# Performance work log

Hardware: AMD Instinct MI355X
Metric: run time of the kernel (lower is better)

The kernel has to match this reference:

```python
import jax, jax.numpy as jnp
import numpy as np

BN_EPS = 1e-5
GRID_W = 17  # conv output width hardcoded via lat_idx*17+lon_idx

def _conv(x, w, b, stride):
    y = jax.lax.conv_general_dilated(x, w, (stride, stride), [(1, 1), (1, 1)],
                                     dimension_numbers=("NCHW", "OIHW", "NCHW"))
    return y + b[None, :, None, None]

def _bn_eval(x, g, b):
    # running_mean=0, running_var=1 (fresh BatchNorm in eval mode)
    inv = jnp.float32(1.0 / np.sqrt(1.0 + BN_EPS))
    return x * (g[None, :, None, None] * inv) + b[None, :, None, None]

def setup_inputs() -> dict:
    key = jax.random.key(0)
    ks = iter(jax.random.split(key, 64))
    def rn(shape, s=0.05):
        return jax.random.normal(next(ks), shape, jnp.float32) * s
    B, S, K = 512, 128, 64
    NR = 100000
    inp = {}
    inp["roads"] = jax.random.randint(next(ks), (B, S), 0, NR)
    inp["ratios"] = jax.random.uniform(next(ks), (B, S), jnp.float32) * 0.9 + 0.1
    inp["T"] = jax.random.normal(next(ks), (1, 1, 138, 138), jnp.float32)
    inp["lon_idx"] = jax.random.randint(next(ks), (B, K), 0, 17)
    inp["lat_idx"] = jax.random.randint(next(ks), (B, K), 0, 17)
    inp["lengths"] = jax.random.uniform(next(ks), (NR,), jnp.float32) * 100.0 + 1.0
    inp["map_u"] = jnp.arange(NR, dtype=jnp.int32)
    inp["map_s1"] = jax.random.randint(next(ks), (NR,), 0, 14)
    inp["map_s2"] = jax.random.randint(next(ks), (NR,), 0, 7)
    inp["map_s3"] = jax.random.randint(next(ks), (NR,), 0, 2)
    inp["emb_u"] = rn((NR, 128))
    inp["emb_s1"] = rn((14, 16)); inp["emb_s2"] = rn((7, 8)); inp["emb_s3"] = rn((2, 4))
    inp["rho_w1"] = rn((156, 512)); inp["rho_b1"] = jnp.zeros((512,), jnp.float32)
    inp["rho_w21"] = rn((512, 128)); inp["rho_b21"] = jnp.zeros((128,), jnp.float32)
    inp["conv1_w"] = rn((32, 1, 5, 5)); inp["conv1_b"] = jnp.zeros((32,), jnp.float32)
    inp["bn1_g"] = jnp.ones((32,), jnp.float32); inp["bn1_b"] = jnp.zeros((32,), jnp.float32)
    inp["conv2_w"] = rn((64, 32, 4, 4)); inp["conv2_b"] = jnp.zeros((64,), jnp.float32)
    inp["bn2_g"] = jnp.ones((64,), jnp.float32); inp["bn2_b"] = jnp.zeros((64,), jnp.float32)
    inp["conv3_w"] = rn((128, 64, 4, 4)); inp["conv3_b"] = jnp.zeros((128,), jnp.float32)
    inp["bn3_g"] = jnp.ones((128,), jnp.float32); inp["bn3_b"] = jnp.zeros((128,), jnp.float32)
    inp["f2_w1"] = rn((128, 256)); inp["f2_b1"] = jnp.zeros((256,), jnp.float32)
    inp["f2_w2"] = rn((256, 128)); inp["f2_b2"] = jnp.zeros((128,), jnp.float32)
    inp["f_w1"] = rn((256, 512)); inp["f_b1"] = jnp.zeros((512,), jnp.float32)
    inp["f_w21"] = rn((512, 1)); inp["f_b21"] = jnp.zeros((1,), jnp.float32)
    inp["f_w22"] = rn((512, 1)); inp["f_b22"] = jnp.zeros((1,), jnp.float32)
    return inp

def reference(roads, ratios, T, lon_idx, lat_idx, lengths, map_u, map_s1, map_s2, map_s3,
              emb_u, emb_s1, emb_s2, emb_s3, rho_w1, rho_b1, rho_w21, rho_b21,
              conv1_w, conv1_b, bn1_g, bn1_b, conv2_w, conv2_b, bn2_g, bn2_b,
              conv3_w, conv3_b, bn3_g, bn3_b, f2_w1, f2_b1, f2_w2, f2_b2,
              f_w1, f_b1, f_w21, f_b21, f_w22, f_b22):
    # road lengths / weights
    road_lens = lengths[roads] * ratios               # (B,S)
    l = road_lens.sum(axis=1)                         # (B,)
    w = road_lens / l[:, None]                        # (B,S)
    # ProbRho (eval: dropout=id, reparameterize -> mu)
    u = emb_u[map_u[roads]]                           # (B,S,128)
    s1 = emb_s1[map_s1[roads]]; s2 = emb_s2[map_s2[roads]]; s3 = emb_s3[map_s3[roads]]
    x = jnp.concatenate([u, s1, s2, s3], axis=2)      # (B,S,156)
    h = jax.nn.relu(x @ rho_w1 + rho_b1)
    rho = h @ rho_w21 + rho_b21                       # (B,S,128)
    # ProbTraffic_spatial conv stack
    t = jax.nn.leaky_relu(_bn_eval(_conv(T, conv1_w, conv1_b, 2), bn1_g, bn1_b), 0.1)
    t = jax.nn.leaky_relu(_bn_eval(_conv(t, conv2_w, conv2_b, 2), bn2_g, bn2_b), 0.1)
    t = jax.nn.leaky_relu(_bn_eval(_conv(t, conv3_w, conv3_b, 2), bn3_g, bn3_b), 0.1)  # (1,128,17,17)
    c_flat = jnp.transpose(t[0], (1, 2, 0)).reshape(-1, t.shape[1])  # (289,128)
    # fused segment gather + mean over each trajectory's grid cells
    idx = lat_idx * GRID_W + lon_idx                  # (B,K)
    c_mean = c_flat[idx].mean(axis=1)                 # (B,128)
    h2 = jax.nn.selu(c_mean @ f2_w1 + f2_b1)
    c2 = h2 @ f2_w2 + f2_b2                           # (B,128)
    # ProbTravelTime
    xcat = jnp.concatenate([rho, jnp.broadcast_to(c2[:, None, :], rho.shape)], axis=2)  # (B,S,256)
    h3 = jax.nn.relu(xcat @ f_w1 + f_b1)              # (B,S,512)
    logm = (h3 @ f_w21 + f_b21)[..., 0]               # (B,S)
    logv = (h3 @ f_w22 + f_b22)[..., 0]
    logw = jnp.log(w)
    logm_agg = jax.nn.logsumexp(logm + logw, axis=1)
    logv_agg = jax.nn.logsumexp(logv + 2.0 * logw, axis=1)
    logl = jnp.log(l)
    logmu = logl - logm_agg
    loglam = logl - 3.0 * logm_agg - logv_agg
    return (logmu, loglam)
```

## Files before the change

kernel.cpp:

```cpp
#include <hip/hip_runtime.h>
#include <hip/hip_bf16.h>
#include <math.h>

#define BB 512
#define SS 128
#define NROWS (BB*SS)
#define TMG 128
#define NBLKG (NROWS/TMG)

__device__ __forceinline__ float leaky01(float x){ return x >= 0.f ? x : 0.1f*x; }

#define BN_INV 0.9999950000374997f
#define SELU_A 1.6732632423543772f
#define SELU_S 1.0507009873554805f

typedef __attribute__((ext_vector_type(8))) short short8;
typedef __attribute__((ext_vector_type(4))) float f32x4;

__device__ __forceinline__ unsigned short f2bf(float f) {
    unsigned int u = __float_as_uint(f);
    u += 0x7fff + ((u >> 16) & 1);
    return (unsigned short)(u >> 16);
}
__device__ __forceinline__ unsigned int pk2(float a, float b) {
    __hip_bfloat162 h = __float22bfloat162_rn(make_float2(a, b));
    unsigned int u;
    __builtin_memcpy(&u, &h, 4);
    return u;
}
__device__ __forceinline__ uint2 pack4bf(float a, float b, float c, float d) {
    uint2 r; r.x = pk2(a, b); r.y = pk2(c, d); return r;
}

__device__ __forceinline__ unsigned short* xsp(unsigned short* base, int row, int col) {
    unsigned off = (unsigned)(row*384 + col*2);
    off ^= (unsigned)((row & 7) << 4);
    return (unsigned short*)((char*)base + off);
}
__device__ __forceinline__ unsigned short* h1p(unsigned short* base, int row, int col) {
    unsigned off = (unsigned)(row*1024 + col*2);
    off ^= (unsigned)((row & 7) << 4);
    return (unsigned short*)((char*)base + off);
}
__device__ __forceinline__ unsigned short* xcp(unsigned short* base, int row, int col) {
    unsigned off = (unsigned)(row*256 + col*2);
    off ^= (unsigned)((row & 7) << 4);
    return (unsigned short*)((char*)base + off);
}

#define PREP_N (278528 + 32768 + 131072)
#define PREP_BLOCKS (PREP_N/256)
#define CONV1_BLOCKS 578

__global__ __launch_bounds__(256) void combo1_kernel(
    const float* __restrict__ w1, const float* __restrict__ w21, const float* __restrict__ fw1,
    unsigned short* __restrict__ sw1, unsigned short* __restrict__ sw21, unsigned short* __restrict__ sw3,
    const float* __restrict__ c2w_in, const float* __restrict__ c3w_in,
    float* __restrict__ w2t, float* __restrict__ w3t,
    const float* __restrict__ T, const float* __restrict__ cw,
    const float* __restrict__ cbias, const float* __restrict__ g,
    const float* __restrict__ bb, float* __restrict__ out)
{
    if (blockIdx.x < PREP_BLOCKS) {
        int t = blockIdx.x*256 + threadIdx.x;
        if (t < 81920) {
            int j = t & 7; int r = t >> 3; int lane = r & 63; r >>= 6;
            int ks = r % 5; int nt = r / 5;
            int n = nt*16 + (lane & 15);
            int k = ks*32 + (lane >> 4)*8 + j;
            float v = (k < 156) ? w1[k*512 + n] : 0.f;
            sw1[t] = f2bf(v);
        } else if (t < 147456) {
            int u = t - 81920;
            int j = u & 7; int r = u >> 3; int lane = r & 63; r >>= 6;
            int ks = r & 15; int nt = r >> 4;
            int d = nt*16 + (lane & 15);
            int k = ks*32 + (lane >> 4)*8 + j;
            sw21[u] = f2bf(w21[k*128 + d]);
        } else if (t < 278528) {
            int u = t - 147456;
            int j = u & 7; int r = u >> 3; int lane = r & 63; r >>= 6;
            int ks = r & 7; int nt = r >> 3;
            int n = nt*16 + (lane & 15);
            int k = ks*32 + (lane >> 4)*8 + j;
            sw3[u] = f2bf(fw1[k*512 + n]);
        } else if (t < 278528 + 32768) {
            int u = t - 278528;
            int oc = u >> 9; int r = u & 511;
            int kk = r >> 5; int ic = r & 31;
            w2t[u] = c2w_in[oc*512 + ic*16 + kk];
        } else {
            int u = t - (278528 + 32768);
            int oc = u >> 10; int r = u & 1023;
            int kk = r >> 6; int ic = r & 63;
            w3t[u] = c3w_in[oc*1024 + ic*16 + kk];
        }
    } else {
        int t = (blockIdx.x - PREP_BLOCKS)*256 + threadIdx.x;
        if (t >= 32*68*68) return;
        int oc  = t & 31;
        int pos = t >> 5;
        int oy = pos / 68, ox = pos % 68;
        float acc = cbias[oc];
        #pragma unroll
        for (int ky=0; ky<5; ++ky) {
            int iy = oy*2 - 1 + ky;
            if (iy < 0 || iy >= 138) continue;
            #pragma unroll
            for (int kx=0; kx<5; ++kx) {
                int ix = ox*2 - 1 + kx;
                if (ix < 0 || ix >= 138) continue;
                acc += cw[oc*25 + ky*5 + kx] * T[iy*138 + ix];
            }
        }
        acc = acc * (g[oc]*BN_INV) + bb[oc];
        out[pos*32 + oc] = leaky01(acc);
    }
}

__global__ __launch_bounds__(256) void conv2_kernel(
    const float* __restrict__ in,
    const float* __restrict__ w2t,
    const float* __restrict__ bias, const float* __restrict__ g,
    const float* __restrict__ bb, float* __restrict__ out)
{
    int gid = blockIdx.x*256 + threadIdx.x;
    if (gid >= 64*34*34*4) return;
    int icg = gid & 3;
    int o   = gid >> 2;
    int oc  = o & 63;
    int pos = o >> 6;
    int oy = pos / 34, ox = pos % 34;
    float acc = 0.f;
    #pragma unroll
    for (int ky=0; ky<4; ++ky) {
        int iy = oy*2 - 1 + ky;
        if (iy < 0 || iy >= 68) continue;
        #pragma unroll
        for (int kx=0; kx<4; ++kx) {
            int ix = ox*2 - 1 + kx;
            if (ix < 0 || ix >= 68) continue;
            const float* ip = &in[(iy*68+ix)*32 + icg*8];
            const float* wp = &w2t[oc*512 + (ky*4+kx)*32 + icg*8];
            float4 i0 = *(const float4*)ip, i1 = *(const float4*)(ip+4);
            float4 w0 = *(const float4*)wp, w1v = *(const float4*)(wp+4);
            acc += i0.x*w0.x + i0.y*w0.y + i0.z*w0.z + i0.w*w0.w
                 + i1.x*w1v.x + i1.y*w1v.y + i1.z*w1v.z + i1.w*w1v.w;
        }
    }
    acc += __shfl_xor(acc, 1, 64);
    acc += __shfl_xor(acc, 2, 64);
    if (icg == 0) {
        acc = (acc + bias[oc]) * (g[oc]*BN_INV) + bb[oc];
        out[pos*64 + oc] = leaky01(acc);
    }
}

__global__ __launch_bounds__(256) void conv3_kernel(
    const float* __restrict__ in,
    const float* __restrict__ w3t,
    const float* __restrict__ bias, const float* __restrict__ g,
    const float* __restrict__ bb, float* __restrict__ outT)
{
    int gid = blockIdx.x*256 + threadIdx.x;
    if (gid >= 128*289*8) return;
    int icg = gid & 7;
    int o   = gid >> 3;
    int oc  = o & 127;
    int pos = o >> 7;
    int oy = pos / 17, ox = pos % 17;
    float acc = 0.f;
    #pragma unroll
    for (int ky=0; ky<4; ++ky) {
        int iy = oy*2 - 1 + ky;
        if (iy < 0 || iy >= 34) continue;
        #pragma unroll
        for (int kx=0; kx<4; ++kx) {
            int ix = ox*2 - 1 + kx;
            if (ix < 0 || ix >= 34) continue;
            const float* ip = &in[(iy*34+ix)*64 + icg*8];
            const float* wp = &w3t[oc*1024 + (ky*4+kx)*64 + icg*8];
            float4 i0 = *(const float4*)ip, i1 = *(const float4*)(ip+4);
            float4 w0 = *(const float4*)wp, w1v = *(const float4*)(wp+4);
            acc += i0.x*w0.x + i0.y*w0.y + i0.z*w0.z + i0.w*w0.w
                 + i1.x*w1v.x + i1.y*w1v.y + i1.z*w1v.z + i1.w*w1v.w;
        }
    }
    acc += __shfl_xor(acc, 1, 64);
    acc += __shfl_xor(acc, 2, 64);
    acc += __shfl_xor(acc, 4, 64);
    if (icg == 0) {
        acc = (acc + bias[oc]) * (g[oc]*BN_INV) + bb[oc];
        outT[pos*128 + oc] = leaky01(acc);
    }
}

__global__ __launch_bounds__(256) void cmh2c2_kernel(
    const float* __restrict__ t3T, const int* __restrict__ lat, const int* __restrict__ lon,
    const float* __restrict__ w1, const float* __restrict__ b1,
    const float* __restrict__ w2, const float* __restrict__ b2,
    const float* __restrict__ fw1, const float* __restrict__ fb1,
    float* __restrict__ cvb)
{
    __shared__ int   ps[64];
    __shared__ float part[256];
    __shared__ float cms[128];
    __shared__ float h2s[256];
    __shared__ float c2s[128];
    const int b = blockIdx.x;
    const int tid = threadIdx.x;
    if (tid < 64) ps[tid] = lat[b*64+tid]*17 + lon[b*64+tid];
    __syncthreads();
    {
        int d = tid & 127, half = tid >> 7;
        float s = 0.f;
        #pragma unroll 8
        for (int k=0; k<32; ++k) s += t3T[ps[half*32+k]*128 + d];
        part[tid] = s;
    }
    __syncthreads();
    if (tid < 128) cms[tid] = (part[tid] + part[tid+128]) * (1.f/64.f);
    __syncthreads();
    {
        float acc = b1[tid];
        #pragma unroll 8
        for (int k=0; k<128; ++k) acc += cms[k] * w1[k*256 + tid];
        h2s[tid] = acc > 0.f ? SELU_S*acc : SELU_S*SELU_A*(expf(acc)-1.f);
    }
    __syncthreads();
    {
        int d = tid & 127, half = tid >> 7;
        float acc = 0.f;
        #pragma unroll 8
        for (int k=0; k<128; ++k) acc += h2s[half*128 + k] * w2[(half*128+k)*128 + d];
        part[tid] = acc;
    }
    __syncthreads();
    if (tid < 128) c2s[tid] = part[tid] + part[tid+128] + b2[tid];
    __syncthreads();
    {
        float a0 = fb1[tid], a1 = fb1[tid + 256];
        #pragma unroll 8
        for (int k=0; k<128; ++k) {
            float c = c2s[k];
            a0 += c * fw1[(128+k)*512 + tid];
            a1 += c * fw1[(128+k)*512 + 256 + tid];
        }
        cvb[b*512 + tid]       = a0;
        cvb[b*512 + 256 + tid] = a1;
    }
}

__global__ __launch_bounds__(1024, 4) void mega_kernel(
    const int* __restrict__ roads, const float* __restrict__ ratios,
    const float* __restrict__ lengths,
    const int* __restrict__ map_u, const int* __restrict__ map_s1,
    const int* __restrict__ map_s2, const int* __restrict__ map_s3,
    const float* __restrict__ emb_u, const float* __restrict__ emb_s1,
    const float* __restrict__ emb_s2, const float* __restrict__ emb_s3,
    const unsigned short* __restrict__ sw1, const float* __restrict__ b1,
    const unsigned short* __restrict__ sw21, const float* __restrict__ b21,
    const unsigned short* __restrict__ sw3, const float* __restrict__ cvb,
    const float* __restrict__ fw21, const float* __restrict__ fb21,
    const float* __restrict__ fw22, const float* __restrict__ fb22,
    float* __restrict__ out)
{
    __shared__ unsigned short buf[65536];
    float* pmv = (float*)buf;
    float* fin = (float*)buf + 4096;

    const int tid  = threadIdx.x;
    const int wid  = tid >> 6;
    const int lane = tid & 63;
    const int lo   = lane & 15;
    const int hi   = lane >> 4;
    const int b    = blockIdx.x;
    const int r0   = b * TMG;
    const int nt2  = wid >> 1;
    const int rh   = wid & 1;

    short8 afp00 = *(const short8*)&sw1[((wid*2+0)*5 + 0)*512 + lane*8];
    short8 afp10 = *(const short8*)&sw1[((wid*2+1)*5 + 0)*512 + lane*8];
    short8 afp01 = *(const short8*)&sw1[((wid*2+0)*5 + 1)*512 + lane*8];
    short8 afp11 = *(const short8*)&sw1[((wid*2+1)*5 + 1)*512 + lane*8];

    {
        int row = tid >> 3, seg = tid & 7;
        int road = roads[r0 + row];
        const float* src = emb_u + (long)map_u[road]*128 + seg*16;
        #pragma unroll
        for (int i=0;i<4;++i) {
            float4 v = *(const float4*)&src[i*4];
            *(uint2*)xsp(buf, row, seg*16 + i*4) = pack4bf(v.x, v.y, v.z, v.w);
        }
    }
    for (int idx = tid; idx < 128*32; idx += 1024) {
        int row = idx >> 5, k2 = idx & 31;
        int road = roads[r0 + row];
        float v;
        if      (k2 < 16) v = emb_s1[map_s1[road]*16 + k2];
        else if (k2 < 24) v = emb_s2[map_s2[road]*8  + (k2-16)];
        else if (k2 < 28) v = emb_s3[map_s3[road]*4  + (k2-24)];
        else              v = 0.f;
        *xsp(buf, row, 128 + k2) = f2bf(v);
    }
    __syncthreads();

    f32x4 acc1[2][8];
    {
        #pragma unroll
        for (int mt=0;mt<2;++mt)
            #pragma unroll
            for (int rg=0;rg<8;++rg) acc1[mt][rg]=(f32x4)(0.f);
        short8 a0c = afp00, a1c = afp10, a0n = afp01, a1n = afp11;
        #pragma unroll
        for (int ks=0; ks<5; ++ks) {
            short8 a0f = a0c, a1f = a1c;
            if (ks < 3) {
                a0f = *(const short8*)&sw1[((wid*2+0)*5 + ks+2)*512 + lane*8];
                a1f = *(const short8*)&sw1[((wid*2+1)*5 + ks+2)*512 + lane*8];
            }
            const int kb = ks*32 + hi*8;
            short8 bf[4];
            #pragma unroll
            for (int rg=0;rg<4;++rg) bf[rg] = *(const short8*)xsp(buf, rg*16+lo, kb);
            #pragma unroll
            for (int rg=0;rg<4;++rg) {
                acc1[0][rg] = __builtin_amdgcn_mfma_f32_16x16x32_bf16(a0c, bf[rg], acc1[0][rg], 0,0,0);
                acc1[1][rg] = __builtin_amdgcn_mfma_f32_16x16x32_bf16(a1c, bf[rg], acc1[1][rg], 0,0,0);
            }
            #pragma unroll
            for (int rg=0;rg<4;++rg) bf[rg] = *(const short8*)xsp(buf, (4+rg)*16+lo, kb);
            #pragma unroll
            for (int rg=0;rg<4;++rg) {
                acc1[0][4+rg] = __builtin_amdgcn_mfma_f32_16x16x32_bf16(a0c, bf[rg], acc1[0][4+rg], 0,0,0);
                acc1[1][4+rg] = __builtin_amdgcn_mfma_f32_16x16x32_bf16(a1c, bf[rg], acc1[1][4+rg], 0,0,0);
            }
            a0c = a0n; a1c = a1n; a0n = a0f; a1n = a1f;
        }
    }
    __syncthreads();

    short8 a2q0, a2q1, a2q2, a2q3;
    {
        a2q0 = *(const short8*)&sw21[(nt2*16 + 0)*512 + lane*8];
        a2q1 = *(const short8*)&sw21[(nt2*16 + 1)*512 + lane*8];
        a2q2 = *(const short8*)&sw21[(nt2*16 + 2)*512 + lane*8];
        a2q3 = *(const short8*)&sw21[(nt2*16 + 3)*512 + lane*8];
        const int n0 = wid * 32;
        #pragma unroll
        for (int mt=0;mt<2;++mt) {
            const int nb = n0 + mt*16 + hi*4;
            float4 bias = *(const float4*)&b1[nb];
            const float* bp = (const float*)&bias;
            #pragma unroll
            for (int rg=0;rg<8;++rg) {
                const float* a = (const float*)&acc1[mt][rg];
                float y0 = fmaxf(a[0]+bp[0], 0.f), y1 = fmaxf(a[1]+bp[1], 0.f);
                float y2 = fmaxf(a[2]+bp[2], 0.f), y3 = fmaxf(a[3]+bp[3], 0.f);
                *(uint2*)h1p(buf, rg*16+lo, nb) = pack4bf(y0,y1,y2,y3);
            }
        }
    }
    __syncthreads();

    f32x4 acc2[4];
    {
        #pragma unroll
        for (int i=0;i<4;++i) acc2[i]=(f32x4)(0.f);
        #pragma unroll
        for (int ks=0; ks<16; ++ks) {
            short8 a_use = a2q0;
            a2q0 = a2q1; a2q1 = a2q2; a2q2 = a2q3;
            if (ks < 12)
                a2q3 = *(const short8*)&sw21[(nt2*16 + ks+4)*512 + lane*8];
            const int kb = ks*32 + hi*8;
            short8 bf[4];
            #pragma unroll
            for (int i=0;i<4;++i) bf[i] = *(const short8*)h1p(buf, (rh*4+i)*16+lo, kb);
            #pragma unroll
            for (int i=0;i<4;++i)
                acc2[i] = __builtin_amdgcn_mfma_f32_16x16x32_bf16(a_use, bf[i], acc2[i], 0,0,0);
        }
    }
    __syncthreads();

    short8 a3c0, a3c1, a3n0, a3n1;
    {
        a3c0 = *(const short8*)&sw3[((wid*2+0)*8 + 0)*512 + lane*8];
        a3c1 = *(const short8*)&sw3[((wid*2+1)*8 + 0)*512 + lane*8];
        a3n0 = *(const short8*)&sw3[((wid*2+0)*8 + 1)*512 + lane*8];
        a3n1 = *(const short8*)&sw3[((wid*2+1)*8 + 1)*512 + lane*8];
        const int nb = nt2*16 + hi*4;
        float4 bias = *(const float4*)&b21[nb];
        const float* bp = (const float*)&bias;
        #pragma unroll
        for (int i=0;i<4;++i) {
            const float* a = (const float*)&acc2[i];
            *(uint2*)xcp(buf, (rh*4+i)*16+lo, nb) =
                pack4bf(a[0]+bp[0], a[1]+bp[1], a[2]+bp[2], a[3]+bp[3]);
        }
    }
    __syncthreads();

    float sm[8], sv[8];
    {
        const int n0 = wid * 32;
        f32x4 acc[2][8];
        #pragma unroll
        for (int mt=0;mt<2;++mt)
            #pragma unroll
            for (int rg=0;rg<8;++rg) acc[mt][rg]=(f32x4)(0.f);
        #pragma unroll
        for (int ks=0; ks<4; ++ks) {
            short8 c0f = a3c0, c1f = a3c1;
            if (ks < 2) {
                c0f = *(const short8*)&sw3[((wid*2+0)*8 + ks+2)*512 + lane*8];
                c1f = *(const short8*)&sw3[((wid*2+1)*8 + ks+2)*512 + lane*8];
            }
            const int kb = ks*32 + hi*8;
            short8 bf[4];
            #pragma unroll
            for (int rg=0;rg<4;++rg) bf[rg] = *(const short8*)xcp(buf, rg*16+lo, kb);
            #pragma unroll
            for (int rg=0;rg<4;++rg) {
                acc[0][rg] = __builtin_amdgcn_mfma_f32_16x16x32_bf16(a3c0, bf[rg], acc[0][rg], 0,0,0);
                acc[1][rg] = __builtin_amdgcn_mfma_f32_16x16x32_bf16(a3c1, bf[rg], acc[1][rg], 0,0,0);
            }
            #pragma unroll
            for (int rg=0;rg<4;++rg) bf[rg] = *(const short8*)xcp(buf, (4+rg)*16+lo, kb);
            #pragma unroll
            for (int rg=0;rg<4;++rg) {
                acc[0][4+rg] = __builtin_amdgcn_mfma_f32_16x16x32_bf16(a3c0, bf[rg], acc[0][4+rg], 0,0,0);
                acc[1][4+rg] = __builtin_amdgcn_mfma_f32_16x16x32_bf16(a3c1, bf[rg], acc[1][4+rg], 0,0,0);
            }
            a3c0 = a3n0; a3c1 = a3n1; a3n0 = c0f; a3n1 = c1f;
        }
        #pragma unroll
        for (int rg=0;rg<8;++rg){ sm[rg]=0.f; sv[rg]=0.f; }
        #pragma unroll
        for (int mt=0;mt<2;++mt) {
            const int nb = n0 + mt*16 + hi*4;
            float4 bias = *(const float4*)&cvb[b*512 + nb];
            float4 wm   = *(const float4*)&fw21[nb];
            float4 wv   = *(const float4*)&fw22[nb];
            const float *bp=(const float*)&bias, *wmp=(const float*)&wm, *wvp=(const float*)&wv;
            #pragma unroll
            for (int rg=0;rg<8;++rg) {
                const float* a = (const float*)&acc[mt][rg];
                #pragma unroll
                for (int j=0;j<4;++j) {
                    float y = fmaxf(a[j]+bp[j], 0.f);
                    sm[rg] += y*wmp[j];
                    sv[rg] += y*wvp[j];
                }
            }
        }
        #pragma unroll
        for (int rg=0;rg<8;++rg) {
            sm[rg] += __shfl_xor(sm[rg], 16, 64); sm[rg] += __shfl_xor(sm[rg], 32, 64);
            sv[rg] += __shfl_xor(sv[rg], 16, 64); sv[rg] += __shfl_xor(sv[rg], 32, 64);
        }
    }
    __syncthreads();
    if (hi == 0) {
        #pragma unroll
        for (int rg=0;rg<8;++rg) {
            pmv[wid*128 + rg*16 + lo]        = sm[rg];
            pmv[2048 + wid*128 + rg*16 + lo] = sv[rg];
        }
    }
    __syncthreads();

    float rl = 0.f, am = 0.f, av = 0.f;
    if (tid < 128) {
        float s_m = 0.f, s_v = 0.f;
        #pragma unroll
        for (int w=0; w<16; ++w) {
            s_m += pmv[w*128 + tid];
            s_v += pmv[2048 + w*128 + tid];
        }
        s_m += fb21[0]; s_v += fb22[0];
        int gi = r0 + tid;
        rl = lengths[roads[gi]] * ratios[gi];
        float ws = rl;
        #pragma unroll
        for (int off=32; off; off>>=1) ws += __shfl_xor(ws, off, 64);
        if (lane == 0) fin[wid] = ws;
        am = s_m; av = s_v;
    }
    __syncthreads();
    if (tid < 128) {
        float l = fin[0] + fin[1];
        float logl = logf(l);
        float lw = logf(rl) - logl;
        am += lw; av += 2.f*lw;
        float mm = am, mv = av;
        #pragma unroll
        for (int off=32; off; off>>=1) { mm = fmaxf(mm, __shfl_xor(mm, off, 64)); mv = fmaxf(mv, __shfl_xor(mv, off, 64)); }
        if (lane == 0) { fin[2+wid] = mm; fin[4+wid] = mv; fin[8+wid] = logl; }
    }
    __syncthreads();
    if (tid < 128) {
        float mm = fmaxf(fin[2], fin[3]);
        float mv = fmaxf(fin[4], fin[5]);
        float se = expf(am - mm), sev = expf(av - mv);
        #pragma unroll
        for (int off=32; off; off>>=1) { se += __shfl_xor(se, off, 64); sev += __shfl_xor(sev, off, 64); }
        if (lane == 0) { fin[10+wid] = se; fin[12+wid] = sev; }
    }
    __syncthreads();
    if (tid == 0) {
        float mm = fmaxf(fin[2], fin[3]);
        float mv = fmaxf(fin[4], fin[5]);
        float lsem = logf(fin[10] + fin[11]) + mm;
        float lsev = logf(fin[12] + fin[13]) + mv;
        float logl = fin[8];
        out[b]       = logl - lsem;
        out[512 + b] = logl - 3.f*lsem - lsev;
    }
}

extern "C" void kernel_launch(void* const* d_in, const int* in_sizes, int n_in,
                              void* d_out, int out_size, void* d_ws, size_t ws_size,
                              hipStream_t stream) {
    const int*   roads   = (const int*)  d_in[0];
    const float* ratios  = (const float*)d_in[1];
    const float* T       = (const float*)d_in[2];
    const int*   lon_idx = (const int*)  d_in[3];
    const int*   lat_idx = (const int*)  d_in[4];
    const float* lengths = (const float*)d_in[5];
    const int*   map_u   = (const int*)  d_in[6];
    const int*   map_s1  = (const int*)  d_in[7];
    const int*   map_s2  = (const int*)  d_in[8];
    const int*   map_s3  = (const int*)  d_in[9];
    const float* emb_u   = (const float*)d_in[10];
    const float* emb_s1  = (const float*)d_in[11];
    const float* emb_s2  = (const float*)d_in[12];
    const float* emb_s3  = (const float*)d_in[13];
    const float* rho_w1  = (const float*)d_in[14];
    const float* rho_b1  = (const float*)d_in[15];
    const float* rho_w21 = (const float*)d_in[16];
    const float* rho_b21 = (const float*)d_in[17];
    const float* conv1_w = (const float*)d_in[18];
    const float* conv1_b = (const float*)d_in[19];
    const float* bn1_g   = (const float*)d_in[20];
    const float* bn1_b   = (const float*)d_in[21];
    const float* conv2_w = (const float*)d_in[22];
    const float* conv2_b = (const float*)d_in[23];
    const float* bn2_g   = (const float*)d_in[24];
    const float* bn2_b   = (const float*)d_in[25];
    const float* conv3_w = (const float*)d_in[26];
    const float* conv3_b = (const float*)d_in[27];
    const float* bn3_g   = (const float*)d_in[28];
    const float* bn3_b   = (const float*)d_in[29];
    const float* f2_w1   = (const float*)d_in[30];
    const float* f2_b1   = (const float*)d_in[31];
    const float* f2_w2   = (const float*)d_in[32];
    const float* f2_b2   = (const float*)d_in[33];
    const float* f_w1    = (const float*)d_in[34];
    const float* f_b1    = (const float*)d_in[35];
    const float* f_w21   = (const float*)d_in[36];
    const float* f_b21   = (const float*)d_in[37];
    const float* f_w22   = (const float*)d_in[38];
    const float* f_b22   = (const float*)d_in[39];

    float* ws    = (float*)d_ws;
    float* t1    = ws;
    float* t2    = t1 + 147968;
    float* t3T   = t2 + 73984;
    float* cvb   = t3T + 36992;
    float* w2t   = cvb + 262144;
    float* w3t   = w2t + 32768;
    unsigned short* sw1  = (unsigned short*)(w3t + 131072);
    unsigned short* sw21 = sw1 + 81920;
    unsigned short* sw3  = sw21 + 65536;

    combo1_kernel<<<PREP_BLOCKS + CONV1_BLOCKS, 256, 0, stream>>>(
        rho_w1, rho_w21, f_w1, sw1, sw21, sw3,
        conv2_w, conv3_w, w2t, w3t,
        T, conv1_w, conv1_b, bn1_g, bn1_b, t1);
    conv2_kernel<<<(64*34*34*4 + 255)/256, 256, 0, stream>>>(t1, w2t, conv2_b, bn2_g, bn2_b, t2);
    conv3_kernel<<<(128*289*8 + 255)/256, 256, 0, stream>>>(t2, w3t, conv3_b, bn3_g, bn3_b, t3T);
    cmh2c2_kernel<<<512, 256, 0, stream>>>(t3T, lat_idx, lon_idx, f2_w1, f2_b1, f2_w2, f2_b2,
                                           f_w1, f_b1, cvb);
    mega_kernel<<<NBLKG, 1024, 0, stream>>>(roads, ratios, lengths,
                                            map_u, map_s1, map_s2, map_s3,
                                            emb_u, emb_s1, emb_s2, emb_s3,
                                            sw1, rho_b1, sw21, rho_b21,
                                            sw3, cvb, f_w21, f_b21, f_w22, f_b22,
                                            (float*)d_out);
}
```

Measured before the change: 117.1 us.

## Fuse conv and context prep kernels into one cooperative kernel with grid syncs

Merges the weight-prep/conv1, conv2, conv3 and context-MLP kernels into a single cooperative kernel of 256 blocks by 512 threads. Grid-stride loops cover each stage, and grid.sync separates the dependent stages. The goal is to remove three kernel launch boundaries and their drain/fill gaps, at the cost of grid-wide barriers and fewer resident threads per conv stage. The change also relaxes mega_kernel's launch-bounds occupancy hint from 4 to 2, which can change its register allocation, and switches embedding gathers to nontemporal loads.

```diff
diff --git a/kernel.cpp b/kernel.cpp
--- a/kernel.cpp
+++ b/kernel.cpp
@@ -1,6 +1,9 @@
 #include <hip/hip_runtime.h>
 #include <hip/hip_bf16.h>
+#include <hip/hip_cooperative_groups.h>
 #include <math.h>
+
+namespace cg = cooperative_groups;
 
 #define BB 512
 #define SS 128
@@ -48,210 +51,213 @@
     return (unsigned short*)((char*)base + off);
 }
 
-#define PREP_N (278528 + 32768 + 131072)
-#define PREP_BLOCKS (PREP_N/256)
-#define CONV1_BLOCKS 578
-
-__global__ __launch_bounds__(256) void combo1_kernel(
+#define PREP_N 442368
+#define C1_N   147968
+#define C2_N   (64*34*34*4)
+#define C3_N   (128*289*8)
+#define GRID_T (256*512)
+
+__global__ __launch_bounds__(512) void fused_pre_kernel(
     const float* __restrict__ w1, const float* __restrict__ w21, const float* __restrict__ fw1,
     unsigned short* __restrict__ sw1, unsigned short* __restrict__ sw21, unsigned short* __restrict__ sw3,
     const float* __restrict__ c2w_in, const float* __restrict__ c3w_in,
     float* __restrict__ w2t, float* __restrict__ w3t,
-    const float* __restrict__ T, const float* __restrict__ cw,
-    const float* __restrict__ cbias, const float* __restrict__ g,
-    const float* __restrict__ bb, float* __restrict__ out)
+    const float* __restrict__ T, const float* __restrict__ c1w,
+    const float* __restrict__ c1b, const float* __restrict__ g1, const float* __restrict__ bb1,
+    float* __restrict__ t1,
+    const float* __restrict__ c2bias, const float* __restrict__ g2, const float* __restrict__ bb2,
+    float* __restrict__ t2,
+    const float* __restrict__ c3bias, const float* __restrict__ g3, const float* __restrict__ bb3,
+    float* __restrict__ t3T,
+    const int* __restrict__ lat, const int* __restrict__ lon,
+    const float* __restrict__ f2w1, const float* __restrict__ f2b1,
+    const float* __restrict__ f2w2, const float* __restrict__ f2b2,
+    const float* __restrict__ fb1, float* __restrict__ cvb)
 {
-    if (blockIdx.x < PREP_BLOCKS) {
-        int t = blockIdx.x*256 + threadIdx.x;
-        if (t < 81920) {
-            int j = t & 7; int r = t >> 3; int lane = r & 63; r >>= 6;
+    cg::grid_group grid = cg::this_grid();
+    const int tid = threadIdx.x;
+    const int gt  = blockIdx.x*512 + tid;
+
+    __shared__ int   pss[128];
+    __shared__ float cms[256];
+    __shared__ float h2s[512];
+    __shared__ float part[512];
+    __shared__ float c2s[256];
+
+    for (int i = gt; i < PREP_N + C1_N; i += GRID_T) {
+        if (i < 81920) {
+            int j = i & 7; int r = i >> 3; int lane = r & 63; r >>= 6;
             int ks = r % 5; int nt = r / 5;
             int n = nt*16 + (lane & 15);
             int k = ks*32 + (lane >> 4)*8 + j;
             float v = (k < 156) ? w1[k*512 + n] : 0.f;
-            sw1[t] = f2bf(v);
-        } else if (t < 147456) {
-            int u = t - 81920;
+            sw1[i] = f2bf(v);
+        } else if (i < 147456) {
+            int u = i - 81920;
             int j = u & 7; int r = u >> 3; int lane = r & 63; r >>= 6;
             int ks = r & 15; int nt = r >> 4;
             int d = nt*16 + (lane & 15);
             int k = ks*32 + (lane >> 4)*8 + j;
             sw21[u] = f2bf(w21[k*128 + d]);
-        } else if (t < 278528) {
-            int u = t - 147456;
+        } else if (i < 278528) {
+            int u = i - 147456;
             int j = u & 7; int r = u >> 3; int lane = r & 63; r >>= 6;
             int ks = r & 7; int nt = r >> 3;
             int n = nt*16 + (lane & 15);
             int k = ks*32 + (lane >> 4)*8 + j;
             sw3[u] = f2bf(fw1[k*512 + n]);
-        } else if (t < 278528 + 32768) {
-            int u = t - 278528;
+        } else if (i < 278528 + 32768) {
+            int u = i - 278528;
             int oc = u >> 9; int r = u & 511;
             int kk = r >> 5; int ic = r & 31;
             w2t[u] = c2w_in[oc*512 + ic*16 + kk];
-        } else {
-            int u = t - (278528 + 32768);
+        } else if (i < PREP_N) {
+            int u = i - (278528 + 32768);
             int oc = u >> 10; int r = u & 1023;
             int kk = r >> 6; int ic = r & 63;
             w3t[u] = c3w_in[oc*1024 + ic*16 + kk];
-        }
-    } else {
-        int t = (blockIdx.x - PREP_BLOCKS)*256 + threadIdx.x;
-        if (t >= 32*68*68) return;
-        int oc  = t & 31;
-        int pos = t >> 5;
-        int oy = pos / 68, ox = pos % 68;
-        float acc = cbias[oc];
-        #pragma unroll
-        for (int ky=0; ky<5; ++ky) {
+        } else {
+            int t = i - PREP_N;
+            int oc  = t & 31;
+            int pos = t >> 5;
+            int oy = pos / 68, ox = pos % 68;
+            float acc = c1b[oc];
+            #pragma unroll
+            for (int ky=0; ky<5; ++ky) {
+                int iy = oy*2 - 1 + ky;
+                if (iy < 0 || iy >= 138) continue;
+                #pragma unroll
+                for (int kx=0; kx<5; ++kx) {
+                    int ix = ox*2 - 1 + kx;
+                    if (ix < 0 || ix >= 138) continue;
+                    acc += c1w[oc*25 + ky*5 + kx] * T[iy*138 + ix];
+                }
+            }
+            acc = acc * (g1[oc]*BN_INV) + bb1[oc];
+            t1[pos*32 + oc] = leaky01(acc);
+        }
+    }
+    grid.sync();
+
+    for (int gid = gt; gid < C2_N; gid += GRID_T) {
+        int icg = gid & 3;
+        int o   = gid >> 2;
+        int oc  = o & 63;
+        int pos = o >> 6;
+        int oy = pos / 34, ox = pos % 34;
+        float acc = 0.f;
+        #pragma unroll
+        for (int ky=0; ky<4; ++ky) {
             int iy = oy*2 - 1 + ky;
-            if (iy < 0 || iy >= 138) continue;
-            #pragma unroll
-            for (int kx=0; kx<5; ++kx) {
+            if (iy < 0 || iy >= 68) continue;
+            #pragma unroll
+            for (int kx=0; kx<4; ++kx) {
                 int ix = ox*2 - 1 + kx;
-                if (ix < 0 || ix >= 138) continue;
-                acc += cw[oc*25 + ky*5 + kx] * T[iy*138 + ix];
-            }
-        }
-        acc = acc * (g[oc]*BN_INV) + bb[oc];
-        out[pos*32 + oc] = leaky01(acc);
-    }
-}
-
-__global__ __launch_bounds__(256) void conv2_kernel(
-    const float* __restrict__ in,
-    const float* __restrict__ w2t,
-    const float* __restrict__ bias, const float* __restrict__ g,
-    const float* __restrict__ bb, float* __restrict__ out)
-{
-    int gid = blockIdx.x*256 + threadIdx.x;
-    if (gid >= 64*34*34*4) return;
-    int icg = gid & 3;
-    int o   = gid >> 2;
-    int oc  = o & 63;
-    int pos = o >> 6;
-    int oy = pos / 34, ox = pos % 34;
-    float acc = 0.f;
-    #pragma unroll
-    for (int ky=0; ky<4; ++ky) {
-        int iy = oy*2 - 1 + ky;
-        if (iy < 0 || iy >= 68) continue;
-        #pragma unroll
-        for (int kx=0; kx<4; ++kx) {
-            int ix = ox*2 - 1 + kx;
-            if (ix < 0 || ix >= 68) continue;
-            const float* ip = &in[(iy*68+ix)*32 + icg*8];
-            const float* wp = &w2t[oc*512 + (ky*4+kx)*32 + icg*8];
-            float4 i0 = *(const float4*)ip, i1 = *(const float4*)(ip+4);
-            float4 w0 = *(const float4*)wp, w1v = *(const float4*)(wp+4);
-            acc += i0.x*w0.x + i0.y*w0.y + i0.z*w0.z + i0.w*w0.w
-                 + i1.x*w1v.x + i1.y*w1v.y + i1.z*w1v.z + i1.w*w1v.w;
-        }
-    }
-    acc += __shfl_xor(acc, 1, 64);
-    acc += __shfl_xor(acc, 2, 64);
-    if (icg == 0) {
-        acc = (acc + bias[oc]) * (g[oc]*BN_INV) + bb[oc];
-        out[pos*64 + oc] = leaky01(acc);
-    }
-}
-
-__global__ __launch_bounds__(256) void conv3_kernel(
-    const float* __restrict__ in,
-    const float* __restrict__ w3t,
-    const float* __restrict__ bias, const float* __restrict__ g,
-    const float* __restrict__ bb, float* __restrict__ outT)
-{
-    int gid = blockIdx.x*256 + threadIdx.x;
-    if (gid >= 128*289*8) return;
-    int icg = gid & 7;
-    int o   = gid >> 3;
-    int oc  = o & 127;
-    int pos = o >> 7;
-    int oy = pos / 17, ox = pos % 17;
-    float acc = 0.f;
-    #pragma unroll
-    for (int ky=0; ky<4; ++ky) {
-        int iy = oy*2 - 1 + ky;
-        if (iy < 0 || iy >= 34) continue;
-        #pragma unroll
-        for (int kx=0; kx<4; ++kx) {
-            int ix = ox*2 - 1 + kx;
-            if (ix < 0 || ix >= 34) continue;
-            const float* ip = &in[(iy*34+ix)*64 + icg*8];
-            const float* wp = &w3t[oc*1024 + (ky*4+kx)*64 + icg*8];
-            float4 i0 = *(const float4*)ip, i1 = *(const float4*)(ip+4);
-            float4 w0 = *(const float4*)wp, w1v = *(const float4*)(wp+4);
-            acc += i0.x*w0.x + i0.y*w0.y + i0.z*w0.z + i0.w*w0.w
-                 + i1.x*w1v.x + i1.y*w1v.y + i1.z*w1v.z + i1.w*w1v.w;
-        }
-    }
-    acc += __shfl_xor(acc, 1, 64);
-    acc += __shfl_xor(acc, 2, 64);
-    acc += __shfl_xor(acc, 4, 64);
-    if (icg == 0) {
-        acc = (acc + bias[oc]) * (g[oc]*BN_INV) + bb[oc];
-        outT[pos*128 + oc] = leaky01(acc);
-    }
-}
-
-__global__ __launch_bounds__(256) void cmh2c2_kernel(
-    const float* __restrict__ t3T, const int* __restrict__ lat, const int* __restrict__ lon,
-    const float* __restrict__ w1, const float* __restrict__ b1,
-    const float* __restrict__ w2, const float* __restrict__ b2,
-    const float* __restrict__ fw1, const float* __restrict__ fb1,
-    float* __restrict__ cvb)
-{
-    __shared__ int   ps[64];
-    __shared__ float part[256];
-    __shared__ float cms[128];
-    __shared__ float h2s[256];
-    __shared__ float c2s[128];
-    const int b = blockIdx.x;
-    const int tid = threadIdx.x;
-    if (tid < 64) ps[tid] = lat[b*64+tid]*17 + lon[b*64+tid];
-    __syncthreads();
+                if (ix < 0 || ix >= 68) continue;
+                const float* ip = &t1[(iy*68+ix)*32 + icg*8];
+                const float* wp = &w2t[oc*512 + (ky*4+kx)*32 + icg*8];
+                float4 i0 = *(const float4*)ip, i1 = *(const float4*)(ip+4);
+                float4 w0 = *(const float4*)wp, w1v = *(const float4*)(wp+4);
+                acc += i0.x*w0.x + i0.y*w0.y + i0.z*w0.z + i0.w*w0.w
+                     + i1.x*w1v.x + i1.y*w1v.y + i1.z*w1v.z + i1.w*w1v.w;
+            }
+        }
+        acc += __shfl_xor(acc, 1, 64);
+        acc += __shfl_xor(acc, 2, 64);
+        if (icg == 0) {
+            acc = (acc + c2bias[oc]) * (g2[oc]*BN_INV) + bb2[oc];
+            t2[pos*64 + oc] = leaky01(acc);
+        }
+    }
+    grid.sync();
+
+    for (int gid = gt; gid < C3_N; gid += GRID_T) {
+        int icg = gid & 7;
+        int o   = gid >> 3;
+        int oc  = o & 127;
+        int pos = o >> 7;
+        int oy = pos / 17, ox = pos % 17;
+        float acc = 0.f;
+        #pragma unroll
+        for (int ky=0; ky<4; ++ky) {
+            int iy = oy*2 - 1 + ky;
+            if (iy < 0 || iy >= 34) continue;
+            #pragma unroll
+            for (int kx=0; kx<4; ++kx) {
+                int ix = ox*2 - 1 + kx;
+                if (ix < 0 || ix >= 34) continue;
+                const float* ip = &t2[(iy*34+ix)*64 + icg*8];
+                const float* wp = &w3t[oc*1024 + (ky*4+kx)*64 + icg*8];
+                float4 i0 = *(const float4*)ip, i1 = *(const float4*)(ip+4);
+                float4 w0 = *(const float4*)wp, w1v = *(const float4*)(wp+4);
+                acc += i0.x*w0.x + i0.y*w0.y + i0.z*w0.z + i0.w*w0.w
+                     + i1.x*w1v.x + i1.y*w1v.y + i1.z*w1v.z + i1.w*w1v.w;
+            }
+        }
+        acc += __shfl_xor(acc, 1, 64);
+        acc += __shfl_xor(acc, 2, 64);
+        acc += __shfl_xor(acc, 4, 64);
+        if (icg == 0) {
+            acc = (acc + c3bias[oc]) * (g3[oc]*BN_INV) + bb3[oc];
+            t3T[pos*128 + oc] = leaky01(acc);
+        }
+    }
+    grid.sync();
+
     {
-        int d = tid & 127, half = tid >> 7;
-        float s = 0.f;
-        #pragma unroll 8
-        for (int k=0; k<32; ++k) s += t3T[ps[half*32+k]*128 + d];
-        part[tid] = s;
-    }
-    __syncthreads();
-    if (tid < 128) cms[tid] = (part[tid] + part[tid+128]) * (1.f/64.f);
-    __syncthreads();
-    {
-        float acc = b1[tid];
-        #pragma unroll 8
-        for (int k=0; k<128; ++k) acc += cms[k] * w1[k*256 + tid];
-        h2s[tid] = acc > 0.f ? SELU_S*acc : SELU_S*SELU_A*(expf(acc)-1.f);
-    }
-    __syncthreads();
-    {
-        int d = tid & 127, half = tid >> 7;
-        float acc = 0.f;
-        #pragma unroll 8
-        for (int k=0; k<128; ++k) acc += h2s[half*128 + k] * w2[(half*128+k)*128 + d];
-        part[tid] = acc;
-    }
-    __syncthreads();
-    if (tid < 128) c2s[tid] = part[tid] + part[tid+128] + b2[tid];
-    __syncthreads();
-    {
-        float a0 = fb1[tid], a1 = fb1[tid + 256];
-        #pragma unroll 8
-        for (int k=0; k<128; ++k) {
-            float c = c2s[k];
-            a0 += c * fw1[(128+k)*512 + tid];
-            a1 += c * fw1[(128+k)*512 + 256 + tid];
-        }
-        cvb[b*512 + tid]       = a0;
-        cvb[b*512 + 256 + tid] = a1;
-    }
-}
-
-__global__ __launch_bounds__(1024, 4) void mega_kernel(
+        const int b0 = blockIdx.x * 2;
+        if (tid < 128) {
+            int bl = tid >> 6, k = tid & 63;
+            pss[tid] = lat[(b0+bl)*64+k]*17 + lon[(b0+bl)*64+k];
+        }
+        __syncthreads();
+        {
+            int half = tid >> 8, r = tid & 255, bl = r >> 7, d = r & 127;
+            float s = 0.f;
+            #pragma unroll 8
+            for (int k=0; k<32; ++k) s += t3T[pss[bl*64 + half*32 + k]*128 + d];
+            part[(bl*2+half)*128 + d] = s;
+        }
+        __syncthreads();
+        if (tid < 256) {
+            int bl = tid >> 7, d = tid & 127;
+            cms[bl*128+d] = (part[(bl*2)*128+d] + part[(bl*2+1)*128+d]) * (1.f/64.f);
+        }
+        __syncthreads();
+        {
+            int bl = tid >> 8, n = tid & 255;
+            float a = f2b1[n];
+            #pragma unroll 8
+            for (int k=0; k<128; ++k) a += cms[bl*128+k] * f2w1[k*256+n];
+            h2s[bl*256+n] = a > 0.f ? SELU_S*a : SELU_S*SELU_A*(expf(a)-1.f);
+        }
+        __syncthreads();
+        {
+            int q = tid >> 7, d = tid & 127, bl = q >> 1, half = q & 1;
+            float a = 0.f;
+            #pragma unroll 8
+            for (int k=0; k<128; ++k) a += h2s[bl*256 + half*128 + k] * f2w2[(half*128+k)*128 + d];
+            part[q*128 + d] = a;
+        }
+        __syncthreads();
+        if (tid < 256) {
+            int bl = tid >> 7, d = tid & 127;
+            c2s[bl*128+d] = part[(bl*2)*128+d] + part[(bl*2+1)*128+d] + f2b2[d];
+        }
+        __syncthreads();
+        #pragma unroll
+        for (int it=0; it<2; ++it) {
+            int idx = tid + it*512;
+            int bl = idx >> 9, n = idx & 511;
+            float a = fb1[n];
+            #pragma unroll 8
+            for (int k=0; k<128; ++k) a += c2s[bl*128+k] * fw1[(128+k)*512 + n];
+            cvb[(b0+bl)*512 + n] = a;
+        }
+    }
+}
+
+__global__ __launch_bounds__(1024, 2) void mega_kernel(
     const int* __restrict__ roads, const float* __restrict__ ratios,
     const float* __restrict__ lengths,
     const int* __restrict__ map_u, const int* __restrict__ map_s1,
@@ -287,10 +293,10 @@
     {
         int row = tid >> 3, seg = tid & 7;
         int road = roads[r0 + row];
-        const float* src = emb_u + (long)map_u[road]*128 + seg*16;
+        const f32x4* src = (const f32x4*)(emb_u + (long)map_u[road]*128 + seg*16);
         #pragma unroll
         for (int i=0;i<4;++i) {
-            float4 v = *(const float4*)&src[i*4];
+            f32x4 v = __builtin_nontemporal_load(&src[i]);
             *(uint2*)xsp(buf, row, seg*16 + i*4) = pack4bf(v.x, v.y, v.z, v.w);
         }
     }
@@ -298,9 +304,9 @@
         int row = idx >> 5, k2 = idx & 31;
         int road = roads[r0 + row];
         float v;
-        if      (k2 < 16) v = emb_s1[map_s1[road]*16 + k2];
-        else if (k2 < 24) v = emb_s2[map_s2[road]*8  + (k2-16)];
-        else if (k2 < 28) v = emb_s3[map_s3[road]*4  + (k2-24)];
+        if      (k2 < 16) v = __builtin_nontemporal_load(&emb_s1[map_s1[road]*16 + k2]);
+        else if (k2 < 24) v = __builtin_nontemporal_load(&emb_s2[map_s2[road]*8  + (k2-16)]);
+        else if (k2 < 28) v = __builtin_nontemporal_load(&emb_s3[map_s3[road]*4  + (k2-24)]);
         else              v = 0.f;
         *xsp(buf, row, 128 + k2) = f2bf(v);
     }
@@ -576,14 +582,20 @@
     unsigned short* sw21 = sw1 + 81920;
     unsigned short* sw3  = sw21 + 65536;
 
-    combo1_kernel<<<PREP_BLOCKS + CONV1_BLOCKS, 256, 0, stream>>>(
-        rho_w1, rho_w21, f_w1, sw1, sw21, sw3,
-        conv2_w, conv3_w, w2t, w3t,
-        T, conv1_w, conv1_b, bn1_g, bn1_b, t1);
-    conv2_kernel<<<(64*34*34*4 + 255)/256, 256, 0, stream>>>(t1, w2t, conv2_b, bn2_g, bn2_b, t2);
-    conv3_kernel<<<(128*289*8 + 255)/256, 256, 0, stream>>>(t2, w3t, conv3_b, bn3_g, bn3_b, t3T);
-    cmh2c2_kernel<<<512, 256, 0, stream>>>(t3T, lat_idx, lon_idx, f2_w1, f2_b1, f2_w2, f2_b2,
-                                           f_w1, f_b1, cvb);
+    void* kargs[] = {
+        (void*)&rho_w1, (void*)&rho_w21, (void*)&f_w1,
+        (void*)&sw1, (void*)&sw21, (void*)&sw3,
+        (void*)&conv2_w, (void*)&conv3_w, (void*)&w2t, (void*)&w3t,
+        (void*)&T, (void*)&conv1_w, (void*)&conv1_b, (void*)&bn1_g, (void*)&bn1_b, (void*)&t1,
+        (void*)&conv2_b, (void*)&bn2_g, (void*)&bn2_b, (void*)&t2,
+        (void*)&conv3_b, (void*)&bn3_g, (void*)&bn3_b, (void*)&t3T,
+        (void*)&lat_idx, (void*)&lon_idx,
+        (void*)&f2_w1, (void*)&f2_b1, (void*)&f2_w2, (void*)&f2_b2,
+        (void*)&f_b1, (void*)&cvb
+    };
+    (void)hipLaunchCooperativeKernel((const void*)fused_pre_kernel, dim3(256), dim3(512),
+                                     kargs, 0, stream);
+
     mega_kernel<<<NBLKG, 1024, 0, stream>>>(roads, ratios, lengths,
                                             map_u, map_s1, map_s2, map_s3,
                                             emb_u, emb_s1, emb_s2, emb_s3,
```

Result: slower. 224.0 us (+91.2%).

## Batch two trajectories per cmh2c2 block, drop syncs, simplify logsumexp epilogue

Applied to the files above, without the earlier changes.

cmh2c2 now handles two trajectories per block, so each weight load from w1, w2 and fw1 is reused for two batch rows and the grid is halved. mega_kernel moves the xc tile to a separate extra shared-memory region, which lets it drop two __syncthreads, at the cost of more LDS per block and a lower launch-bound occupancy hint. The final logsumexp reduction is rewritten algebraically as plain sums of rl*exp(logm) and rl^2*exp(logv), which removes several reduction passes and barriers. That form drops the max subtraction, so it can overflow or lose precision if the logits are large.

```diff
diff --git a/kernel.cpp b/kernel.cpp
--- a/kernel.cpp
+++ b/kernel.cpp
@@ -42,10 +42,10 @@
     off ^= (unsigned)((row & 7) << 4);
     return (unsigned short*)((char*)base + off);
 }
-__device__ __forceinline__ unsigned short* xcp(unsigned short* base, int row, int col) {
+__device__ __forceinline__ unsigned short* xcq(unsigned short* xbase, int row, int col) {
     unsigned off = (unsigned)(row*256 + col*2);
     off ^= (unsigned)((row & 7) << 4);
-    return (unsigned short*)((char*)base + off);
+    return (unsigned short*)((char*)xbase + off);
 }
 
 #define PREP_N (278528 + 32768 + 131072)
@@ -202,56 +202,65 @@
     const float* __restrict__ fw1, const float* __restrict__ fb1,
     float* __restrict__ cvb)
 {
-    __shared__ int   ps[64];
-    __shared__ float part[256];
-    __shared__ float cms[128];
-    __shared__ float h2s[256];
-    __shared__ float c2s[128];
-    const int b = blockIdx.x;
+    __shared__ int   ps[128];
+    __shared__ float cms[256];
+    __shared__ float h2s[512];
+    __shared__ float c2s[256];
+    const int b0 = blockIdx.x * 2;
     const int tid = threadIdx.x;
-    if (tid < 64) ps[tid] = lat[b*64+tid]*17 + lon[b*64+tid];
-    __syncthreads();
-    {
-        int d = tid & 127, half = tid >> 7;
+    if (tid < 128) {
+        int bl = tid >> 6, k = tid & 63;
+        ps[tid] = lat[(b0+bl)*64+k]*17 + lon[(b0+bl)*64+k];
+    }
+    __syncthreads();
+    {
+        int bl = tid >> 7, d = tid & 127;
         float s = 0.f;
         #pragma unroll 8
-        for (int k=0; k<32; ++k) s += t3T[ps[half*32+k]*128 + d];
-        part[tid] = s;
-    }
-    __syncthreads();
-    if (tid < 128) cms[tid] = (part[tid] + part[tid+128]) * (1.f/64.f);
-    __syncthreads();
-    {
-        float acc = b1[tid];
-        #pragma unroll 8
-        for (int k=0; k<128; ++k) acc += cms[k] * w1[k*256 + tid];
-        h2s[tid] = acc > 0.f ? SELU_S*acc : SELU_S*SELU_A*(expf(acc)-1.f);
-    }
-    __syncthreads();
-    {
-        int d = tid & 127, half = tid >> 7;
-        float acc = 0.f;
-        #pragma unroll 8
-        for (int k=0; k<128; ++k) acc += h2s[half*128 + k] * w2[(half*128+k)*128 + d];
-        part[tid] = acc;
-    }
-    __syncthreads();
-    if (tid < 128) c2s[tid] = part[tid] + part[tid+128] + b2[tid];
-    __syncthreads();
-    {
-        float a0 = fb1[tid], a1 = fb1[tid + 256];
-        #pragma unroll 8
+        for (int k=0; k<64; ++k) s += t3T[ps[bl*64+k]*128 + d];
+        cms[tid] = s * (1.f/64.f);
+    }
+    __syncthreads();
+    {
+        float bb0 = b1[tid];
+        float a0 = bb0, a1 = bb0;
+        #pragma unroll 4
         for (int k=0; k<128; ++k) {
-            float c = c2s[k];
-            a0 += c * fw1[(128+k)*512 + tid];
-            a1 += c * fw1[(128+k)*512 + 256 + tid];
-        }
-        cvb[b*512 + tid]       = a0;
-        cvb[b*512 + 256 + tid] = a1;
-    }
-}
-
-__global__ __launch_bounds__(1024, 4) void mega_kernel(
+            float w = w1[k*256 + tid];
+            a0 += cms[k] * w;
+            a1 += cms[128+k] * w;
+        }
+        h2s[tid]       = a0 > 0.f ? SELU_S*a0 : SELU_S*SELU_A*(expf(a0)-1.f);
+        h2s[256 + tid] = a1 > 0.f ? SELU_S*a1 : SELU_S*SELU_A*(expf(a1)-1.f);
+    }
+    __syncthreads();
+    {
+        int bl = tid >> 7, d = tid & 127;
+        float a = 0.f;
+        #pragma unroll 4
+        for (int k=0; k<256; ++k) a += h2s[bl*256 + k] * w2[k*128 + d];
+        c2s[bl*128 + d] = a + b2[d];
+    }
+    __syncthreads();
+    {
+        float f0 = fb1[tid], f1 = fb1[tid + 256];
+        float a00 = f0, a01 = f1, a10 = f0, a11 = f1;
+        #pragma unroll 4
+        for (int k=0; k<128; ++k) {
+            float w0 = fw1[(128+k)*512 + tid];
+            float w1v= fw1[(128+k)*512 + 256 + tid];
+            float c0 = c2s[k], c1 = c2s[128+k];
+            a00 += c0*w0; a01 += c0*w1v;
+            a10 += c1*w0; a11 += c1*w1v;
+        }
+        cvb[b0*512 + tid]             = a00;
+        cvb[b0*512 + 256 + tid]       = a01;
+        cvb[(b0+1)*512 + tid]         = a10;
+        cvb[(b0+1)*512 + 256 + tid]   = a11;
+    }
+}
+
+__global__ __launch_bounds__(1024, 2) void mega_kernel(
     const int* __restrict__ roads, const float* __restrict__ ratios,
     const float* __restrict__ lengths,
     const int* __restrict__ map_u, const int* __restrict__ map_s1,
@@ -265,7 +274,8 @@
     const float* __restrict__ fw22, const float* __restrict__ fb22,
     float* __restrict__ out)
 {
-    __shared__ unsigned short buf[65536];
+    __shared__ unsigned short buf[81920];
+    unsigned short* xcs = buf + 65536;
     float* pmv = (float*)buf;
     float* fin = (float*)buf + 4096;
 
@@ -383,7 +393,6 @@
                 acc2[i] = __builtin_amdgcn_mfma_f32_16x16x32_bf16(a_use, bf[i], acc2[i], 0,0,0);
         }
     }
-    __syncthreads();
 
     short8 a3c0, a3c1, a3n0, a3n1;
     {
@@ -397,7 +406,7 @@
         #pragma unroll
         for (int i=0;i<4;++i) {
             const float* a = (const float*)&acc2[i];
-            *(uint2*)xcp(buf, (rh*4+i)*16+lo, nb) =
+            *(uint2*)xcq(xcs, (rh*4+i)*16+lo, nb) =
                 pack4bf(a[0]+bp[0], a[1]+bp[1], a[2]+bp[2], a[3]+bp[3]);
         }
     }
@@ -421,14 +430,14 @@
             const int kb = ks*32 + hi*8;
             short8 bf[4];
             #pragma unroll
-            for (int rg=0;rg<4;++rg) bf[rg] = *(const short8*)xcp(buf, rg*16+lo, kb);
+            for (int rg=0;rg<4;++rg) bf[rg] = *(const short8*)xcq(xcs, rg*16+lo, kb);
             #pragma unroll
             for (int rg=0;rg<4;++rg) {
                 acc[0][rg] = __builtin_amdgcn_mfma_f32_16x16x32_bf16(a3c0, bf[rg], acc[0][rg], 0,0,0);
                 acc[1][rg] = __builtin_amdgcn_mfma_f32_16x16x32_bf16(a3c1, bf[rg], acc[1][rg], 0,0,0);
             }
             #pragma unroll
-            for (int rg=0;rg<4;++rg) bf[rg] = *(const short8*)xcp(buf, (4+rg)*16+lo, kb);
+            for (int rg=0;rg<4;++rg) bf[rg] = *(const short8*)xcq(xcs, (4+rg)*16+lo, kb);
             #pragma unroll
             for (int rg=0;rg<4;++rg) {
                 acc[0][4+rg] = __builtin_amdgcn_mfma_f32_16x16x32_bf16(a3c0, bf[rg], acc[0][4+rg], 0,0,0);
@@ -462,7 +471,6 @@
             sv[rg] += __shfl_xor(sv[rg], 16, 64); sv[rg] += __shfl_xor(sv[rg], 32, 64);
         }
     }
-    __syncthreads();
     if (hi == 0) {
         #pragma unroll
         for (int rg=0;rg<8;++rg) {
@@ -472,7 +480,6 @@
     }
     __syncthreads();
 
-    float rl = 0.f, am = 0.f, av = 0.f;
     if (tid < 128) {
         float s_m = 0.f, s_v = 0.f;
         #pragma unroll
@@ -482,42 +489,26 @@
         }
         s_m += fb21[0]; s_v += fb22[0];
         int gi = r0 + tid;
-        rl = lengths[roads[gi]] * ratios[gi];
-        float ws = rl;
-        #pragma unroll
-        for (int off=32; off; off>>=1) ws += __shfl_xor(ws, off, 64);
-        if (lane == 0) fin[wid] = ws;
-        am = s_m; av = s_v;
-    }
-    __syncthreads();
-    if (tid < 128) {
-        float l = fin[0] + fin[1];
-        float logl = logf(l);
-        float lw = logf(rl) - logl;
-        am += lw; av += 2.f*lw;
-        float mm = am, mv = av;
-        #pragma unroll
-        for (int off=32; off; off>>=1) { mm = fmaxf(mm, __shfl_xor(mm, off, 64)); mv = fmaxf(mv, __shfl_xor(mv, off, 64)); }
-        if (lane == 0) { fin[2+wid] = mm; fin[4+wid] = mv; fin[8+wid] = logl; }
-    }
-    __syncthreads();
-    if (tid < 128) {
-        float mm = fmaxf(fin[2], fin[3]);
-        float mv = fmaxf(fin[4], fin[5]);
-        float se = expf(am - mm), sev = expf(av - mv);
-        #pragma unroll
-        for (int off=32; off; off>>=1) { se += __shfl_xor(se, off, 64); sev += __shfl_xor(sev, off, 64); }
-        if (lane == 0) { fin[10+wid] = se; fin[12+wid] = sev; }
+        float rl = lengths[roads[gi]] * ratios[gi];
+        float pl = rl;
+        float p1 = rl * expf(s_m);
+        float p2 = rl * rl * expf(s_v);
+        #pragma unroll
+        for (int off=32; off; off>>=1) {
+            pl += __shfl_xor(pl, off, 64);
+            p1 += __shfl_xor(p1, off, 64);
+            p2 += __shfl_xor(p2, off, 64);
+        }
+        if (lane == 0) { fin[wid*4+0] = pl; fin[wid*4+1] = p1; fin[wid*4+2] = p2; }
     }
     __syncthreads();
     if (tid == 0) {
-        float mm = fmaxf(fin[2], fin[3]);
-        float mv = fmaxf(fin[4], fin[5]);
-        float lsem = logf(fin[10] + fin[11]) + mm;
-        float lsev = logf(fin[12] + fin[13]) + mv;
-        float logl = fin[8];
-        out[b]       = logl - lsem;
-        out[512 + b] = logl - 3.f*lsem - lsev;
+        float L  = fin[0] + fin[4];
+        float S1 = fin[1] + fin[5];
+        float S2 = fin[2] + fin[6];
+        float logl = logf(L), ls1 = logf(S1), ls2 = logf(S2);
+        out[b]       = 2.f*logl - ls1;
+        out[512 + b] = 6.f*logl - 3.f*ls1 - ls2;
     }
 }
 
@@ -582,7 +573,7 @@
         T, conv1_w, conv1_b, bn1_g, bn1_b, t1);
     conv2_kernel<<<(64*34*34*4 + 255)/256, 256, 0, stream>>>(t1, w2t, conv2_b, bn2_g, bn2_b, t2);
     conv3_kernel<<<(128*289*8 + 255)/256, 256, 0, stream>>>(t2, w3t, conv3_b, bn3_g, bn3_b, t3T);
-    cmh2c2_kernel<<<512, 256, 0, stream>>>(t3T, lat_idx, lon_idx, f2_w1, f2_b1, f2_w2, f2_b2,
+    cmh2c2_kernel<<<256, 256, 0, stream>>>(t3T, lat_idx, lon_idx, f2_w1, f2_b1, f2_w2, f2_b2,
                                            f_w1, f_b1, cvb);
     mega_kernel<<<NBLKG, 1024, 0, stream>>>(roads, ratios, lengths,
                                             map_u, map_s1, map_s2, map_s3,
```

Measured after the change: 136.3 us. 16.3% more time.
